# Kernel tuning notes

Hardware: AMD Instinct MI355X
Metric: run time of the kernel (lower is better)

Reference implementation:

```python
import jax, jax.numpy as jnp
import numpy as np


def _hausdorff(x, y):
    # x, y: [B, C, N, D] point sets per (batch, channel); rows are points.
    x2 = jnp.sum(x * x, axis=-1)                       # [B, C, N]
    y2 = jnp.sum(y * y, axis=-1)                       # [B, C, M]
    xy = jnp.einsum('bcnd,bcmd->bcnm', x, y)           # [B, C, N, M]
    d2 = x2[..., :, None] + y2[..., None, :] - 2.0 * xy
    d = jnp.sqrt(jnp.maximum(d2, 0.0))                 # Euclidean distances
    d_fwd = jnp.max(jnp.min(d, axis=-1), axis=-1)      # max_n min_m, [B, C]
    d_bwd = jnp.max(jnp.min(d, axis=-2), axis=-1)      # max_m min_n, [B, C]
    return jnp.maximum(d_fwd, d_bwd)                   # symmetric Hausdorff [B, C]


def setup_inputs() -> dict:
    key = jax.random.key(0)
    k1, k2 = jax.random.split(key)
    B, C, H, W = 8, 3, 1024, 1024
    inp = jax.random.normal(k1, (B, C, H, W), dtype=jnp.float32)
    tgt = jax.random.normal(k2, (B, C, H, W), dtype=jnp.float32)
    return {'input': inp, 'target': tgt}


def reference(input, target):
    h = _hausdorff(input, target)        # [B, C]
    # original: sum_i mean_c(h[i]) / B == mean over (B, C)
    return jnp.mean(h)
```

## Files before the change

### kernel.cpp

```cpp
#include <hip/hip_runtime.h>
#include <math.h>

constexpr int BC = 24;
constexpr int N  = 1024;
constexpr int D  = 1024;
constexpr int TILE = 128;
constexpr int BK = 64;
constexpr int SKF = 40;

typedef short short8 __attribute__((ext_vector_type(8)));
typedef float f32x4  __attribute__((ext_vector_type(4)));

#define FINF 3.402823466e+38f

#define GLDS16(g, l)                                                          \
    __builtin_amdgcn_global_load_lds(                                         \
        (const __attribute__((address_space(1))) void*)(g),                   \
        (__attribute__((address_space(3))) void*)(l), 16, 0, 0)

__device__ inline unsigned pk_bf16(float a, float b) {
    unsigned ua = __float_as_uint(a) + 0x8000u;
    unsigned ub = __float_as_uint(b) + 0x8000u;
    return __builtin_amdgcn_perm(ub, ua, 0x07060302);
}

__global__ __launch_bounds__(256) void prep_kernel(const float* __restrict__ X,
                                                   const float* __restrict__ Y,
                                                   unsigned short* __restrict__ Xbf,
                                                   unsigned short* __restrict__ Ybf,
                                                   float* __restrict__ xn,
                                                   float* __restrict__ yn,
                                                   unsigned* __restrict__ minbuf,
                                                   float* __restrict__ out) {
    if (blockIdx.x < 2 * BC * N / 256) {
        minbuf[blockIdx.x * 256 + threadIdx.x] = 0xFFFFFFFFu;
        if (blockIdx.x == 0 && threadIdx.x == 0) *out = 0.f;
    }
    int w = threadIdx.x >> 6, lane = threadIdx.x & 63;
    #pragma unroll
    for (int it = 0; it < 4; it++) {
        long rid = (long)blockIdx.x * 4 + w + (long)it * 12288;
        bool isY = rid >= (long)BC * N;
        long row = isY ? rid - (long)BC * N : rid;
        const float* src = (isY ? Y : X) + row * D;
        unsigned short* dst = (isY ? Ybf : Xbf) + row * D;
        float s = 0.f;
        #pragma unroll
        for (int q = 0; q < 2; q++) {
            float4 a = *(const float4*)(src + lane * 8 + q * 512);
            float4 b = *(const float4*)(src + lane * 8 + q * 512 + 4);
            s += a.x * a.x + a.y * a.y + a.z * a.z + a.w * a.w;
            s += b.x * b.x + b.y * b.y + b.z * b.z + b.w * b.w;
            uint4 pk;
            pk.x = pk_bf16(a.x, a.y); pk.y = pk_bf16(a.z, a.w);
            pk.z = pk_bf16(b.x, b.y); pk.w = pk_bf16(b.z, b.w);
            ((uint4*)dst)[lane + q * 64] = pk;
        }
        #pragma unroll
        for (int m = 1; m < 64; m <<= 1) s += __shfl_xor(s, m, 64);
        if (lane == 0) (isY ? yn : xn)[row] = s;
    }
}

__global__ __launch_bounds__(256) void tile_bf16_kernel(const unsigned short* __restrict__ Xbf,
                                                        const unsigned short* __restrict__ Ybf,
                                                        const float* __restrict__ xn,
                                                        const float* __restrict__ yn,
                                                        unsigned* __restrict__ rowmin,
                                                        unsigned* __restrict__ colmin) {
    __shared__ unsigned short Xs[TILE * BK];
    __shared__ unsigned short Ys[TILE * BK];
    int bc = blockIdx.z, tn = blockIdx.y, tm = blockIdx.x;
    const unsigned short* Xb = Xbf + ((size_t)bc * N + (size_t)tn * TILE) * D;
    const unsigned short* Yb = Ybf + ((size_t)bc * N + (size_t)tm * TILE) * D;

    int t = threadIdx.x;
    int wave = t >> 6, lane = t & 63;
    int wr = wave >> 1, wc = wave & 1;
    int quad = lane >> 4, tx = lane & 15;

    const unsigned short* gx[4];
    const unsigned short* gy[4];
    #pragma unroll
    for (int i = 0; i < 4; i++) {
        int p = t + 256 * i;
        int row = p >> 3;
        int kc = (p & 7) ^ ((p >> 4) & 7);
        gx[i] = Xb + (size_t)row * D + kc * 8;
        gy[i] = Yb + (size_t)row * D + kc * 8;
    }

    f32x4 acc[4][4];
    #pragma unroll
    for (int i = 0; i < 4; i++)
        #pragma unroll
        for (int j = 0; j < 4; j++) acc[i][j] = (f32x4)0.f;

    int aoff[2][4], boff[2][4];
    #pragma unroll
    for (int kh = 0; kh < 2; kh++) {
        #pragma unroll
        for (int mi = 0; mi < 4; mi++) {
            int ra = wr * 64 + mi * 16 + tx;
            aoff[kh][mi] = (ra * 8 + ((kh * 4 + quad) ^ ((ra >> 1) & 7))) * 8;
            int rb = wc * 64 + mi * 16 + tx;
            boff[kh][mi] = (rb * 8 + ((kh * 4 + quad) ^ ((rb >> 1) & 7))) * 8;
        }
    }

    for (int k0 = 0; k0 < D; k0 += BK) {
        __syncthreads();
        #pragma unroll
        for (int i = 0; i < 4; i++) {
            GLDS16(gx[i] + k0, &Xs[(t + 256 * i) * 8]);
            GLDS16(gy[i] + k0, &Ys[(t + 256 * i) * 8]);
        }
        __syncthreads();

        #pragma unroll
        for (int kh = 0; kh < 2; kh++) {
            short8 af[4], bg[4];
            #pragma unroll
            for (int mi = 0; mi < 4; mi++) af[mi] = *(const short8*)&Xs[aoff[kh][mi]];
            #pragma unroll
            for (int mj = 0; mj < 4; mj++) bg[mj] = *(const short8*)&Ys[boff[kh][mj]];
            #pragma unroll
            for (int mi = 0; mi < 4; mi++)
                #pragma unroll
                for (int mj = 0; mj < 4; mj++)
                    acc[mi][mj] = __builtin_amdgcn_mfma_f32_16x16x32_bf16(af[mi], bg[mj], acc[mi][mj], 0, 0, 0);
        }
    }

    int rbase = bc * N + tn * TILE + wr * 64;
    int cbase = bc * N + tm * TILE + wc * 64;
    float xnr[4][4], ynr[4];
    #pragma unroll
    for (int mi = 0; mi < 4; mi++)
        #pragma unroll
        for (int r = 0; r < 4; r++) xnr[mi][r] = xn[rbase + mi * 16 + quad * 4 + r];
    #pragma unroll
    for (int mj = 0; mj < 4; mj++) ynr[mj] = yn[cbase + mj * 16 + tx];

    float rmin[4][4], cmin[4];
    #pragma unroll
    for (int mi = 0; mi < 4; mi++)
        #pragma unroll
        for (int r = 0; r < 4; r++) rmin[mi][r] = FINF;
    #pragma unroll
    for (int mj = 0; mj < 4; mj++) cmin[mj] = FINF;

    #pragma unroll
    for (int mi = 0; mi < 4; mi++)
        #pragma unroll
        for (int mj = 0; mj < 4; mj++)
            #pragma unroll
            for (int r = 0; r < 4; r++) {
                float d2 = fmaxf(xnr[mi][r] + ynr[mj] - 2.f * acc[mi][mj][r], 0.f);
                rmin[mi][r] = fminf(rmin[mi][r], d2);
                cmin[mj]    = fminf(cmin[mj], d2);
            }

    #pragma unroll
    for (int m = 1; m < 16; m <<= 1)
        #pragma unroll
        for (int mi = 0; mi < 4; mi++)
            #pragma unroll
            for (int r = 0; r < 4; r++)
                rmin[mi][r] = fminf(rmin[mi][r], __shfl_xor(rmin[mi][r], m, 64));
    if (tx == 0) {
        #pragma unroll
        for (int mi = 0; mi < 4; mi++)
            #pragma unroll
            for (int r = 0; r < 4; r++)
                atomicMin(&rowmin[rbase + mi * 16 + quad * 4 + r], __float_as_uint(rmin[mi][r]));
    }
    #pragma unroll
    for (int m = 16; m < 64; m <<= 1)
        #pragma unroll
        for (int mj = 0; mj < 4; mj++)
            cmin[mj] = fminf(cmin[mj], __shfl_xor(cmin[mj], m, 64));
    if (quad == 0) {
        #pragma unroll
        for (int mj = 0; mj < 4; mj++)
            atomicMin(&colmin[cbase + mj * 16 + tx], __float_as_uint(cmin[mj]));
    }
}

__global__ __launch_bounds__(256) void norms_kernel(const float* __restrict__ X,
                                                    const float* __restrict__ Y,
                                                    float* __restrict__ xn,
                                                    float* __restrict__ yn) {
    int w = threadIdx.x >> 6, lane = threadIdx.x & 63;
    long rid = (long)blockIdx.x * 4 + w;
    bool isY = rid >= (long)BC * N;
    long row = isY ? rid - (long)BC * N : rid;
    const float* src = (isY ? Y : X) + row * D;
    float s = 0.f;
    #pragma unroll
    for (int q = 0; q < 4; q++) {
        float4 v = ((const float4*)src)[lane + q * 64];
        s += v.x * v.x + v.y * v.y + v.z * v.z + v.w * v.w;
    }
    #pragma unroll
    for (int m = 1; m < 64; m <<= 1) s += __shfl_xor(s, m, 64);
    if (lane == 0) (isY ? yn : xn)[row] = s;
}

__global__ __launch_bounds__(256) void tile_conv_kernel(const float* __restrict__ X,
                                                        const float* __restrict__ Y,
                                                        const float* __restrict__ xn,
                                                        const float* __restrict__ yn,
                                                        unsigned* __restrict__ rowmin,
                                                        unsigned* __restrict__ colmin) {
    __shared__ unsigned short Xs[TILE * SKF];
    __shared__ unsigned short Ys[TILE * SKF];
    int bc = blockIdx.z, tn = blockIdx.y, tm = blockIdx.x;
    const float* Xb = X + ((size_t)bc * N + (size_t)tn * TILE) * D;
    const float* Yb = Y + ((size_t)bc * N + (size_t)tm * TILE) * D;

    int t = threadIdx.x;
    int srow = t >> 3, sq = t & 7;
    int wave = t >> 6, lane = t & 63;
    int wr = wave >> 1, wc = wave & 1;
    int quad = lane >> 4, tx = lane & 15;

    f32x4 acc[4][4];
    #pragma unroll
    for (int i = 0; i < 4; i++)
        #pragma unroll
        for (int j = 0; j < 4; j++) acc[i][j] = (f32x4)0.f;

    float4 xv[4], yv[4];
    #pragma unroll
    for (int i = 0; i < 4; i++) {
        xv[i] = *(const float4*)(Xb + (size_t)(srow + i * 32) * D + sq * 4);
        yv[i] = *(const float4*)(Yb + (size_t)(srow + i * 32) * D + sq * 4);
    }

    for (int k0 = 0; k0 < D; k0 += 32) {
        __syncthreads();
        #pragma unroll
        for (int i = 0; i < 4; i++) {
            uint2 px; px.x = pk_bf16(xv[i].x, xv[i].y); px.y = pk_bf16(xv[i].z, xv[i].w);
            *(uint2*)&Xs[(srow + i * 32) * SKF + sq * 4] = px;
            uint2 py; py.x = pk_bf16(yv[i].x, yv[i].y); py.y = pk_bf16(yv[i].z, yv[i].w);
            *(uint2*)&Ys[(srow + i * 32) * SKF + sq * 4] = py;
        }
        __syncthreads();
        if (k0 + 32 < D) {
            #pragma unroll
            for (int i = 0; i < 4; i++) {
                xv[i] = *(const float4*)(Xb + (size_t)(srow + i * 32) * D + k0 + 32 + sq * 4);
                yv[i] = *(const float4*)(Yb + (size_t)(srow + i * 32) * D + k0 + 32 + sq * 4);
            }
        }
        short8 af[4], bg[4];
        #pragma unroll
        for (int mi = 0; mi < 4; mi++)
            af[mi] = *(const short8*)&Xs[(wr * 64 + mi * 16 + tx) * SKF + quad * 8];
        #pragma unroll
        for (int mj = 0; mj < 4; mj++)
            bg[mj] = *(const short8*)&Ys[(wc * 64 + mj * 16 + tx) * SKF + quad * 8];
        #pragma unroll
        for (int mi = 0; mi < 4; mi++)
            #pragma unroll
            for (int mj = 0; mj < 4; mj++)
                acc[mi][mj] = __builtin_amdgcn_mfma_f32_16x16x32_bf16(af[mi], bg[mj], acc[mi][mj], 0, 0, 0);
    }

    int rbase = bc * N + tn * TILE + wr * 64;
    int cbase = bc * N + tm * TILE + wc * 64;
    float xnr[4][4], ynr[4];
    #pragma unroll
    for (int mi = 0; mi < 4; mi++)
        #pragma unroll
        for (int r = 0; r < 4; r++) xnr[mi][r] = xn[rbase + mi * 16 + quad * 4 + r];
    #pragma unroll
    for (int mj = 0; mj < 4; mj++) ynr[mj] = yn[cbase + mj * 16 + tx];

    float rmin[4][4], cmin[4];
    #pragma unroll
    for (int mi = 0; mi < 4; mi++)
        #pragma unroll
        for (int r = 0; r < 4; r++) rmin[mi][r] = FINF;
    #pragma unroll
    for (int mj = 0; mj < 4; mj++) cmin[mj] = FINF;

    #pragma unroll
    for (int mi = 0; mi < 4; mi++)
        #pragma unroll
        for (int mj = 0; mj < 4; mj++)
            #pragma unroll
            for (int r = 0; r < 4; r++) {
                float d2 = fmaxf(xnr[mi][r] + ynr[mj] - 2.f * acc[mi][mj][r], 0.f);
                rmin[mi][r] = fminf(rmin[mi][r], d2);
                cmin[mj]    = fminf(cmin[mj], d2);
            }

    #pragma unroll
    for (int m = 1; m < 16; m <<= 1)
        #pragma unroll
        for (int mi = 0; mi < 4; mi++)
            #pragma unroll
            for (int r = 0; r < 4; r++)
                rmin[mi][r] = fminf(rmin[mi][r], __shfl_xor(rmin[mi][r], m, 64));
    if (tx == 0) {
        #pragma unroll
        for (int mi = 0; mi < 4; mi++)
            #pragma unroll
            for (int r = 0; r < 4; r++)
                atomicMin(&rowmin[rbase + mi * 16 + quad * 4 + r], __float_as_uint(rmin[mi][r]));
    }
    #pragma unroll
    for (int m = 16; m < 64; m <<= 1)
        #pragma unroll
        for (int mj = 0; mj < 4; mj++)
            cmin[mj] = fminf(cmin[mj], __shfl_xor(cmin[mj], m, 64));
    if (quad == 0) {
        #pragma unroll
        for (int mj = 0; mj < 4; mj++)
            atomicMin(&colmin[cbase + mj * 16 + tx], __float_as_uint(cmin[mj]));
    }
}

__global__ __launch_bounds__(256) void finalize_kernel(const unsigned* __restrict__ rowmin,
                                                       const unsigned* __restrict__ colmin,
                                                       float* __restrict__ out) {
    int bc = blockIdx.x;
    float v = 0.f;
    for (int i = threadIdx.x; i < N; i += 256) {
        v = fmaxf(v, __uint_as_float(rowmin[bc * N + i]));
        v = fmaxf(v, __uint_as_float(colmin[bc * N + i]));
    }
    #pragma unroll
    for (int m = 1; m < 64; m <<= 1) v = fmaxf(v, __shfl_xor(v, m, 64));
    __shared__ float ws[4];
    int lane = threadIdx.x & 63, w = threadIdx.x >> 6;
    if (lane == 0) ws[w] = v;
    __syncthreads();
    if (threadIdx.x == 0) {
        float m = fmaxf(fmaxf(ws[0], ws[1]), fmaxf(ws[2], ws[3]));
        atomicAdd(out, sqrtf(m) * (1.0f / (float)BC));
    }
}

extern "C" void kernel_launch(void* const* d_in, const int* in_sizes, int n_in,
                              void* d_out, int out_size, void* d_ws, size_t ws_size,
                              hipStream_t stream) {
    const float* X = (const float*)d_in[0];
    const float* Y = (const float*)d_in[1];
    float* out = (float*)d_out;

    unsigned* rowmin = (unsigned*)d_ws;
    unsigned* colmin = rowmin + BC * N;
    float* xn = (float*)(colmin + BC * N);
    float* yn = xn + BC * N;
    size_t head = (size_t)4 * BC * N * 4;
    size_t bf_bytes = (size_t)BC * N * D * 2;

    dim3 grid(N / TILE, N / TILE, BC);
    if (ws_size >= head + 2 * bf_bytes) {
        unsigned short* Xbf = (unsigned short*)((char*)d_ws + head);
        unsigned short* Ybf = Xbf + (size_t)BC * N * D;
        prep_kernel<<<3072, 256, 0, stream>>>(X, Y, Xbf, Ybf, xn, yn, rowmin, out);
        tile_bf16_kernel<<<grid, 256, 0, stream>>>(Xbf, Ybf, xn, yn, rowmin, colmin);
    } else {
        hipMemsetAsync(d_ws, 0xFF, (size_t)2 * BC * N * sizeof(unsigned), stream);
        hipMemsetAsync(d_out, 0, sizeof(float), stream);
        norms_kernel<<<2 * BC * N / 4, 256, 0, stream>>>(X, Y, xn, yn);
        tile_conv_kernel<<<grid, 256, 0, stream>>>(X, Y, xn, yn, rowmin, colmin);
    }
    finalize_kernel<<<BC, 256, 0, stream>>>(rowmin, colmin, out);
}
```

Measured before the change: 299.7 us.

## Pre-swizzle bf16 operands into MFMA fragment layout and drop LDS staging

The prep kernel now writes bf16 data in a 16x32 fragment-tiled layout, so each wave loads its MFMA operands straight from global memory with one 16-byte load per lane. The GEMM kernel no longer uses LDS or __syncthreads and double-buffers its fragment loads in registers. Block IDs are remapped so each XCD works on a contiguous set of batch-channels, which should improve L2 reuse. Row norms are now built with atomics after memsets. The cost is that operand reuse now depends on L2 rather than shared memory, which may add global traffic, and there are extra memset launches.

```diff
diff --git a/kernel.cpp b/kernel.cpp
--- a/kernel.cpp
+++ b/kernel.cpp
@@ -5,7 +5,6 @@
 constexpr int N  = 1024;
 constexpr int D  = 1024;
 constexpr int TILE = 128;
-constexpr int BK = 64;
 constexpr int SKF = 40;
 
 typedef short short8 __attribute__((ext_vector_type(8)));
@@ -13,10 +12,6 @@
 
 #define FINF 3.402823466e+38f
 
-#define GLDS16(g, l)                                                          \
-    __builtin_amdgcn_global_load_lds(                                         \
-        (const __attribute__((address_space(1))) void*)(g),                   \
-        (__attribute__((address_space(3))) void*)(l), 16, 0, 0)
 
 __device__ inline unsigned pk_bf16(float a, float b) {
     unsigned ua = __float_as_uint(a) + 0x8000u;
@@ -26,69 +21,57 @@
 
 __global__ __launch_bounds__(256) void prep_kernel(const float* __restrict__ X,
                                                    const float* __restrict__ Y,
-                                                   unsigned short* __restrict__ Xbf,
-                                                   unsigned short* __restrict__ Ybf,
+                                                   unsigned short* __restrict__ Xsw,
+                                                   unsigned short* __restrict__ Ysw,
                                                    float* __restrict__ xn,
-                                                   float* __restrict__ yn,
-                                                   unsigned* __restrict__ minbuf,
-                                                   float* __restrict__ out) {
-    if (blockIdx.x < 2 * BC * N / 256) {
-        minbuf[blockIdx.x * 256 + threadIdx.x] = 0xFFFFFFFFu;
-        if (blockIdx.x == 0 && threadIdx.x == 0) *out = 0.f;
-    }
-    int w = threadIdx.x >> 6, lane = threadIdx.x & 63;
-    #pragma unroll
-    for (int it = 0; it < 4; it++) {
-        long rid = (long)blockIdx.x * 4 + w + (long)it * 12288;
-        bool isY = rid >= (long)BC * N;
-        long row = isY ? rid - (long)BC * N : rid;
-        const float* src = (isY ? Y : X) + row * D;
-        unsigned short* dst = (isY ? Ybf : Xbf) + row * D;
-        float s = 0.f;
-        #pragma unroll
-        for (int q = 0; q < 2; q++) {
-            float4 a = *(const float4*)(src + lane * 8 + q * 512);
-            float4 b = *(const float4*)(src + lane * 8 + q * 512 + 4);
-            s += a.x * a.x + a.y * a.y + a.z * a.z + a.w * a.w;
-            s += b.x * b.x + b.y * b.y + b.z * b.z + b.w * b.w;
-            uint4 pk;
-            pk.x = pk_bf16(a.x, a.y); pk.y = pk_bf16(a.z, a.w);
-            pk.z = pk_bf16(b.x, b.y); pk.w = pk_bf16(b.z, b.w);
-            ((uint4*)dst)[lane + q * 64] = pk;
-        }
-        #pragma unroll
-        for (int m = 1; m < 64; m <<= 1) s += __shfl_xor(s, m, 64);
-        if (lane == 0) (isY ? yn : xn)[row] = s;
-    }
-}
-
-__global__ __launch_bounds__(256) void tile_bf16_kernel(const unsigned short* __restrict__ Xbf,
-                                                        const unsigned short* __restrict__ Ybf,
+                                                   float* __restrict__ yn) {
+    int wave = threadIdx.x >> 6, lane = threadIdx.x & 63;
+    int gtile = blockIdx.x * 4 + wave;
+    bool isY = gtile >= 49152;
+    int tile = isY ? gtile - 49152 : gtile;
+    int bc = tile >> 11;
+    int rk = tile & 2047;
+    int R = rk >> 5, K = rk & 31;
+    int r16 = lane & 15, quad = lane >> 4;
+
+    const float* src = (isY ? Y : X) + ((size_t)bc * N + R * 16 + r16) * D + K * 32 + quad * 8;
+    float4 a = *(const float4*)src;
+    float4 b = *(const float4*)(src + 4);
+
+    uint4 pk;
+    pk.x = pk_bf16(a.x, a.y); pk.y = pk_bf16(a.z, a.w);
+    pk.z = pk_bf16(b.x, b.y); pk.w = pk_bf16(b.z, b.w);
+    unsigned short* dst = (isY ? Ysw : Xsw) + (size_t)tile * 512 + lane * 8;
+    *(uint4*)dst = pk;
+
+    float s = a.x * a.x + a.y * a.y + a.z * a.z + a.w * a.w
+            + b.x * b.x + b.y * b.y + b.z * b.z + b.w * b.w;
+    s += __shfl_xor(s, 16, 64);
+    s += __shfl_xor(s, 32, 64);
+    if (quad == 0)
+        atomicAdd(&(isY ? yn : xn)[bc * N + R * 16 + r16], s);
+}
+
+__global__ __launch_bounds__(256) void tile_bf16_kernel(const unsigned short* __restrict__ Xsw,
+                                                        const unsigned short* __restrict__ Ysw,
                                                         const float* __restrict__ xn,
                                                         const float* __restrict__ yn,
                                                         unsigned* __restrict__ rowmin,
                                                         unsigned* __restrict__ colmin) {
-    __shared__ unsigned short Xs[TILE * BK];
-    __shared__ unsigned short Ys[TILE * BK];
-    int bc = blockIdx.z, tn = blockIdx.y, tm = blockIdx.x;
-    const unsigned short* Xb = Xbf + ((size_t)bc * N + (size_t)tn * TILE) * D;
-    const unsigned short* Yb = Ybf + ((size_t)bc * N + (size_t)tm * TILE) * D;
-
-    int t = threadIdx.x;
-    int wave = t >> 6, lane = t & 63;
+    int id = blockIdx.x;
+    int xcd = id & 7, q = id >> 3;
+    int bc = xcd * 3 + (q >> 6);
+    int txy = q & 63;
+    int tm = txy & 7, tn = txy >> 3;
+
+    int wave = threadIdx.x >> 6, lane = threadIdx.x & 63;
     int wr = wave >> 1, wc = wave & 1;
     int quad = lane >> 4, tx = lane & 15;
 
-    const unsigned short* gx[4];
-    const unsigned short* gy[4];
-    #pragma unroll
-    for (int i = 0; i < 4; i++) {
-        int p = t + 256 * i;
-        int row = p >> 3;
-        int kc = (p & 7) ^ ((p >> 4) & 7);
-        gx[i] = Xb + (size_t)row * D + kc * 8;
-        gy[i] = Yb + (size_t)row * D + kc * 8;
-    }
+    const unsigned short* Xb = Xsw + (size_t)bc * 2048 * 512;
+    const unsigned short* Yb = Ysw + (size_t)bc * 2048 * 512;
+    const unsigned short* ax = Xb + (size_t)(tn * 8 + wr * 4) * 32 * 512 + lane * 8;
+    const unsigned short* by = Yb + (size_t)(tm * 8 + wc * 4) * 32 * 512 + lane * 8;
 
     f32x4 acc[4][4];
     #pragma unroll
@@ -96,40 +79,27 @@
         #pragma unroll
         for (int j = 0; j < 4; j++) acc[i][j] = (f32x4)0.f;
 
-    int aoff[2][4], boff[2][4];
-    #pragma unroll
-    for (int kh = 0; kh < 2; kh++) {
-        #pragma unroll
-        for (int mi = 0; mi < 4; mi++) {
-            int ra = wr * 64 + mi * 16 + tx;
-            aoff[kh][mi] = (ra * 8 + ((kh * 4 + quad) ^ ((ra >> 1) & 7))) * 8;
-            int rb = wc * 64 + mi * 16 + tx;
-            boff[kh][mi] = (rb * 8 + ((kh * 4 + quad) ^ ((rb >> 1) & 7))) * 8;
+    short8 af[2][4], bg[2][4];
+    #pragma unroll
+    for (int mi = 0; mi < 4; mi++) {
+        af[0][mi] = *(const short8*)(ax + mi * 16384);
+        bg[0][mi] = *(const short8*)(by + mi * 16384);
+    }
+    #pragma unroll 2
+    for (int d = 0; d < 32; d++) {
+        int cur = d & 1, nxt = cur ^ 1;
+        if (d < 31) {
+            #pragma unroll
+            for (int mi = 0; mi < 4; mi++) {
+                af[nxt][mi] = *(const short8*)(ax + mi * 16384 + (d + 1) * 512);
+                bg[nxt][mi] = *(const short8*)(by + mi * 16384 + (d + 1) * 512);
+            }
         }
-    }
-
-    for (int k0 = 0; k0 < D; k0 += BK) {
-        __syncthreads();
-        #pragma unroll
-        for (int i = 0; i < 4; i++) {
-            GLDS16(gx[i] + k0, &Xs[(t + 256 * i) * 8]);
-            GLDS16(gy[i] + k0, &Ys[(t + 256 * i) * 8]);
-        }
-        __syncthreads();
-
-        #pragma unroll
-        for (int kh = 0; kh < 2; kh++) {
-            short8 af[4], bg[4];
-            #pragma unroll
-            for (int mi = 0; mi < 4; mi++) af[mi] = *(const short8*)&Xs[aoff[kh][mi]];
-            #pragma unroll
-            for (int mj = 0; mj < 4; mj++) bg[mj] = *(const short8*)&Ys[boff[kh][mj]];
-            #pragma unroll
-            for (int mi = 0; mi < 4; mi++)
-                #pragma unroll
-                for (int mj = 0; mj < 4; mj++)
-                    acc[mi][mj] = __builtin_amdgcn_mfma_f32_16x16x32_bf16(af[mi], bg[mj], acc[mi][mj], 0, 0, 0);
-        }
+        #pragma unroll
+        for (int mi = 0; mi < 4; mi++)
+            #pragma unroll
+            for (int mj = 0; mj < 4; mj++)
+                acc[mi][mj] = __builtin_amdgcn_mfma_f32_16x16x32_bf16(af[cur][mi], bg[cur][mj], acc[mi][mj], 0, 0, 0);
     }
 
     int rbase = bc * N + tn * TILE + wr * 64;
@@ -359,15 +329,18 @@
     size_t head = (size_t)4 * BC * N * 4;
     size_t bf_bytes = (size_t)BC * N * D * 2;
 
-    dim3 grid(N / TILE, N / TILE, BC);
     if (ws_size >= head + 2 * bf_bytes) {
-        unsigned short* Xbf = (unsigned short*)((char*)d_ws + head);
-        unsigned short* Ybf = Xbf + (size_t)BC * N * D;
-        prep_kernel<<<3072, 256, 0, stream>>>(X, Y, Xbf, Ybf, xn, yn, rowmin, out);
-        tile_bf16_kernel<<<grid, 256, 0, stream>>>(Xbf, Ybf, xn, yn, rowmin, colmin);
+        unsigned short* Xsw = (unsigned short*)((char*)d_ws + head);
+        unsigned short* Ysw = Xsw + (size_t)BC * N * D;
+        hipMemsetAsync(d_ws, 0xFF, (size_t)2 * BC * N * 4, stream);
+        hipMemsetAsync(xn, 0, (size_t)2 * BC * N * 4, stream);
+        hipMemsetAsync(d_out, 0, sizeof(float), stream);
+        prep_kernel<<<24576, 256, 0, stream>>>(X, Y, Xsw, Ysw, xn, yn);
+        tile_bf16_kernel<<<1536, 256, 0, stream>>>(Xsw, Ysw, xn, yn, rowmin, colmin);
     } else {
-        hipMemsetAsync(d_ws, 0xFF, (size_t)2 * BC * N * sizeof(unsigned), stream);
+        hipMemsetAsync(d_ws, 0xFF, (size_t)2 * BC * N * 4, stream);
         hipMemsetAsync(d_out, 0, sizeof(float), stream);
+        dim3 grid(N / TILE, N / TILE, BC);
         norms_kernel<<<2 * BC * N / 4, 256, 0, stream>>>(X, Y, xn, yn);
         tile_conv_kernel<<<grid, 256, 0, stream>>>(X, Y, xn, yn, rowmin, colmin);
     }
```

Measured after the change: 303.0 us. No clear change (+1.1%).
